# Kernel tuning notes

Hardware: AMD Instinct MI355X
Metric: run time of the kernel (lower is better)

The kernel has to match this reference:

```python
import jax, jax.numpy as jnp
import numpy as np

D = 1024
H = 16
DH = D // H  # 64
EPS = 1e-5


def _ln(x, w, b=None):
    mu = jnp.mean(x, axis=-1, keepdims=True)
    var = jnp.var(x, axis=-1, keepdims=True)
    y = (x - mu) * jax.lax.rsqrt(var + EPS) * w
    return y + b if b is not None else y


def _rotate_half(x):
    x1, x2 = jnp.split(x, 2, axis=-1)
    return jnp.concatenate([-x2, x1], axis=-1)


def _rope(q, k):
    # q, k: [B, L, H, DH]; rotary over sequence dim (ESM-style half-split rotation)
    L = q.shape[1]
    inv_freq = 1.0 / (10000.0 ** (jnp.arange(0, DH, 2, dtype=jnp.float32) / DH))
    freqs = jnp.arange(L, dtype=jnp.float32)[:, None] * inv_freq[None, :]  # [L, DH/2]
    emb = jnp.concatenate([freqs, freqs], axis=-1)  # [L, DH]
    cos = jnp.cos(emb)[None, :, None, :]  # [1, L, 1, DH]
    sin = jnp.sin(emb)[None, :, None, :]
    q = q * cos + _rotate_half(q) * sin
    k = k * cos + _rotate_half(k) * sin
    return q, k


def setup_inputs() -> dict:
    key = jax.random.key(0)
    ks = jax.random.split(key, 8)
    B, L = 2, 2048
    x = jax.random.normal(ks[0], (B, L, D), dtype=jnp.float32)
    seq_id = jnp.sort(jax.random.randint(ks[1], (B, L), 0, 8), axis=-1)
    s = 1.0 / np.sqrt(D)
    return {
        "x": x,
        "seq_id": seq_id,
        "ln1_w": jnp.ones((D,), jnp.float32),
        "ln1_b": jnp.zeros((D,), jnp.float32),
        "w_qkv": jax.random.normal(ks[2], (3 * D, D), dtype=jnp.float32) * s,
        "q_ln_w": jnp.ones((D,), jnp.float32),
        "k_ln_w": jnp.ones((D,), jnp.float32),
        "out_w": jax.random.normal(ks[3], (D, D), dtype=jnp.float32) * s,
    }


def reference(x, seq_id, ln1_w, ln1_b, w_qkv, q_ln_w, k_ln_w, out_w):
    B, L, _ = x.shape
    h = _ln(x, ln1_w, ln1_b)
    qkv = jnp.einsum("bld,ed->ble", h, w_qkv)  # [B, L, 3D]
    q, k, v = jnp.split(qkv, 3, axis=-1)
    q = _ln(q, q_ln_w)
    k = _ln(k, k_ln_w)
    q = q.reshape(B, L, H, DH)
    k = k.reshape(B, L, H, DH)
    q, k = _rope(q, k)
    q = q.transpose(0, 2, 1, 3)  # [B, H, L, DH]
    k = k.transpose(0, 2, 1, 3)
    v = v.reshape(B, L, H, DH).transpose(0, 2, 1, 3)
    scale = 1.0 / np.sqrt(DH)
    scores = jnp.einsum("bhld,bhmd->bhlm", q, k) * scale  # [B, H, L, L]
    mask = (seq_id[:, None, :, None] == seq_id[:, None, None, :])  # [B, 1, L, L]
    scores = jnp.where(mask, scores, -jnp.inf)
    attn = jax.nn.softmax(scores, axis=-1)
    ctx = jnp.einsum("bhlm,bhmd->bhld", attn, v)  # [B, H, L, DH]
    ctx = ctx.transpose(0, 2, 1, 3).reshape(B, L, D)
    return jnp.einsum("bld,ed->ble", ctx, out_w)
```

## Files before the change

kernel.cpp:

```cpp
#include <hip/hip_runtime.h>
#include <hip/hip_bf16.h>
#include <math.h>

#define D 1024
#define H 16
#define DH 64
#define L 2048
#define B 2
#define NROW (B * L)
#define EPS 1e-5f

typedef _Float16 half8 __attribute__((ext_vector_type(8)));
typedef _Float16 half4v __attribute__((ext_vector_type(4)));
typedef float f32x4 __attribute__((ext_vector_type(4)));

__global__ __launch_bounds__(256) void prep_kernel(const float* __restrict__ x,
                                                   const float* __restrict__ lw,
                                                   const float* __restrict__ lb,
                                                   _Float16* __restrict__ h16,
                                                   const float* __restrict__ wqkv,
                                                   _Float16* __restrict__ wqkv16,
                                                   const float* __restrict__ outw,
                                                   _Float16* __restrict__ outw16,
                                                   const int* __restrict__ seq_id,
                                                   int* __restrict__ lo,
                                                   int* __restrict__ hi,
                                                   float2* __restrict__ rtab) {
    int blk = blockIdx.x;
    int t = threadIdx.x;
    if (blk < 4096) {
        int r = blk;
        const float* xr = x + (size_t)r * D;
        float4 v = *(const float4*)&xr[t * 4];
        float s = v.x + v.y + v.z + v.w;
        float sq = v.x * v.x + v.y * v.y + v.z * v.z + v.w * v.w;
        for (int off = 32; off > 0; off >>= 1) {
            s += __shfl_xor(s, off, 64);
            sq += __shfl_xor(sq, off, 64);
        }
        __shared__ float ls[4], lq[4];
        int wave = t >> 6;
        if ((t & 63) == 0) { ls[wave] = s; lq[wave] = sq; }
        __syncthreads();
        float S = ls[0] + ls[1] + ls[2] + ls[3];
        float Q = lq[0] + lq[1] + lq[2] + lq[3];
        float mu = S / (float)D;
        float rs = rsqrtf(Q / (float)D - mu * mu + EPS);
        float4 w4 = *(const float4*)&lw[t * 4];
        float4 b4 = *(const float4*)&lb[t * 4];
        half4v o = {(_Float16)((v.x - mu) * rs * w4.x + b4.x),
                    (_Float16)((v.y - mu) * rs * w4.y + b4.y),
                    (_Float16)((v.z - mu) * rs * w4.z + b4.z),
                    (_Float16)((v.w - mu) * rs * w4.w + b4.w)};
        *(half4v*)&h16[(size_t)r * D + t * 4] = o;
    } else if (blk < 6144) {
        int base = blk - 4096;
        const float* src;
        _Float16* dst;
        if (base < 1536) { src = wqkv; dst = wqkv16; }
        else             { src = outw; dst = outw16; base -= 1536; }
        int i = (base * 256 + t) * 8;
        float4 a = *(const float4*)&src[i];
        float4 b = *(const float4*)&src[i + 4];
        half8 h = {(_Float16)a.x, (_Float16)a.y, (_Float16)a.z, (_Float16)a.w,
                   (_Float16)b.x, (_Float16)b.y, (_Float16)b.z, (_Float16)b.w};
        *(half8*)&dst[i] = h;
    } else if (blk < 6160) {
        int idx = (blk - 6144) * 256 + t;
        int b = idx / L, l = idx - b * L;
        const int* row = seq_id + (size_t)b * L;
        int v = row[l];
        int a = 0, c = L;
        while (a < c) { int m = (a + c) >> 1; if (row[m] < v) a = m + 1; else c = m; }
        lo[idx] = a;
        a = 0; c = L;
        while (a < c) { int m = (a + c) >> 1; if (row[m] <= v) a = m + 1; else c = m; }
        hi[idx] = a;
    } else {
        int idx = (blk - 6160) * 256 + t;
        int l = idx >> 5, fi = idx & 31;
        float invf = expf(-(float)fi * 0.28782313662425572f);
        float sn, cs;
        sincosf((float)l * invf, &sn, &cs);
        rtab[idx] = make_float2(cs, sn);
    }
}

#define LDA_HALF(BUF, MH, DST)                                                      \
    _Pragma("unroll") for (int mt = 0; mt < 4; mt++) {                              \
        int row_ = mw + (MH) * 64 + mt * 16 + col;                                  \
        _Pragma("unroll") for (int kk = 0; kk < 2; kk++)                            \
            DST[mt][kk] = *(const half8*)&As[BUF][row_][((kk * 4 + quad) ^ (row_ & 7)) * 8]; \
    }

#define LDB_HALF(BUF, NH, DST)                                                      \
    _Pragma("unroll") for (int nt = 0; nt < 2; nt++) {                              \
        int row_ = nw + (NH) * 32 + nt * 16 + col;                                  \
        _Pragma("unroll") for (int kk = 0; kk < 2; kk++)                            \
            DST[nt][kk] = *(const half8*)&Bs[BUF][row_][((kk * 4 + quad) ^ (row_ & 7)) * 8]; \
    }

#define MMA_QUAD(MH, NH, AF, BF)                                                    \
    __builtin_amdgcn_s_setprio(1);                                                  \
    _Pragma("unroll") for (int mt = 0; mt < 4; mt++)                                \
    _Pragma("unroll") for (int nt = 0; nt < 2; nt++) {                              \
        acc[(MH) * 4 + mt][(NH) * 2 + nt] = __builtin_amdgcn_mfma_f32_16x16x32_f16( \
            AF[mt][0], BF[nt][0], acc[(MH) * 4 + mt][(NH) * 2 + nt], 0, 0, 0);      \
        acc[(MH) * 4 + mt][(NH) * 2 + nt] = __builtin_amdgcn_mfma_f32_16x16x32_f16( \
            AF[mt][1], BF[nt][1], acc[(MH) * 4 + mt][(NH) * 2 + nt], 0, 0, 0);      \
    }                                                                               \
    __builtin_amdgcn_s_setprio(0);

__global__ __launch_bounds__(512, 2) void gemm1_8phase(const _Float16* __restrict__ A,
                                                       const _Float16* __restrict__ W,
                                                       _Float16* __restrict__ C,
                                                       _Float16* __restrict__ v_t) {
    __shared__ _Float16 As[2][256][64];
    __shared__ _Float16 Bs[2][256][64];
    int t = threadIdx.x;
    int w = t >> 6, lane = t & 63;
    int quad = lane >> 4, col = lane & 15;

    int i = blockIdx.y * 12 + blockIdx.x;
    int xcd = i & 7, j = i >> 3;
    int tm = (xcd >> 1) * 4 + j / 6;
    int tn = (xcd & 1) * 6 + j % 6;
    int m0 = tm * 256, n0 = tn * 256;
    int mw = (w >> 2) * 128, nw = (w & 3) * 64;

    f32x4 acc[8][4] = {};

    auto stageA = [&](int kt, int buf, int half) {
#pragma unroll
        for (int ii = 0; ii < 2; ii++) {
            int e = half * 1024 + ii * 512 + t;
            int row = e >> 3, ch = e & 7;
            int sch = ch ^ (row & 7);
            __builtin_amdgcn_global_load_lds(
                (const __attribute__((address_space(1))) void*)&A[(size_t)(m0 + row) * 1024 + kt * 64 + sch * 8],
                (__attribute__((address_space(3))) void*)&As[buf][row][ch * 8], 16, 0, 0);
        }
    };
    auto stageB = [&](int kt, int buf, int half) {
#pragma unroll
        for (int ii = 0; ii < 2; ii++) {
            int e = half * 1024 + ii * 512 + t;
            int row = e >> 3, ch = e & 7;
            int sch = ch ^ (row & 7);
            __builtin_amdgcn_global_load_lds(
                (const __attribute__((address_space(1))) void*)&W[(size_t)(n0 + row) * 1024 + kt * 64 + sch * 8],
                (__attribute__((address_space(3))) void*)&Bs[buf][row][ch * 8], 16, 0, 0);
        }
    };

    stageA(0, 0, 0); stageA(0, 0, 1); stageB(0, 0, 0); stageB(0, 0, 1);
    stageA(1, 1, 0);
    asm volatile("s_waitcnt vmcnt(2)" ::: "memory");
    __builtin_amdgcn_s_barrier();

    half8 af[4][2], bf0[2][2], bf1[2][2];
    for (int kt = 0; kt < 16; kt++) {
        int p = kt & 1, np = p ^ 1;

        LDA_HALF(p, 0, af);
        LDB_HALF(p, 0, bf0);
        if (kt + 1 < 16) stageA(kt + 1, np, 1);
        __builtin_amdgcn_s_barrier();
        MMA_QUAD(0, 0, af, bf0);
        __builtin_amdgcn_s_barrier();

        LDB_HALF(p, 1, bf1);
        if (kt + 1 < 16) stageB(kt + 1, np, 0);
        __builtin_amdgcn_s_barrier();
        MMA_QUAD(0, 1, af, bf1);
        __builtin_amdgcn_s_barrier();

        LDA_HALF(p, 1, af);
        if (kt + 1 < 16) stageB(kt + 1, np, 1);
        __builtin_amdgcn_s_barrier();
        MMA_QUAD(1, 1, af, bf1);
        __builtin_amdgcn_s_barrier();

        if (kt + 2 < 16) stageA(kt + 2, p, 0);
        MMA_QUAD(1, 0, af, bf0);
        if (kt < 14)       { asm volatile("s_waitcnt vmcnt(2)" ::: "memory"); }
        else if (kt == 14) { asm volatile("s_waitcnt vmcnt(0)" ::: "memory"); }
        if (kt < 15) __builtin_amdgcn_s_barrier();
    }

    if (n0 >= 2048) {
        int b = m0 >> 11;
#pragma unroll
        for (int mt = 0; mt < 8; mt++)
#pragma unroll
            for (int nt = 0; nt < 4; nt++) {
                int vcol = n0 - 2048 + nw + nt * 16 + col;
                int bh = b * H + (vcol >> 6);
                int d = vcol & 63;
                int l = (m0 & (L - 1)) + mw + mt * 16 + quad * 4;
                half4v pk = {(_Float16)acc[mt][nt][0], (_Float16)acc[mt][nt][1],
                             (_Float16)acc[mt][nt][2], (_Float16)acc[mt][nt][3]};
                *(half4v*)&v_t[((size_t)(bh * 64 + d)) * 2048 + l] = pk;
            }
    } else {
#pragma unroll
        for (int mt = 0; mt < 8; mt++)
#pragma unroll
            for (int nt = 0; nt < 4; nt++)
#pragma unroll
                for (int r = 0; r < 4; r++) {
                    int row = m0 + mw + mt * 16 + quad * 4 + r;
                    int cc = n0 + nw + nt * 16 + col;
                    C[(size_t)row * 3072 + cc] = (_Float16)acc[mt][nt][r];
                }
    }
}

template <typename OutT, int BM, int BN>
__global__ __launch_bounds__(256) void gemm_f16_kernel(const _Float16* __restrict__ A,
                                                       const _Float16* __restrict__ W,
                                                       OutT* __restrict__ C, int N) {
    constexpr int WM = BM / 2, WN = BN / 2;
    constexpr int MT = WM / 16, NT = WN / 16;
    __shared__ _Float16 As[2][BM * 32];
    __shared__ _Float16 Bs[2][BN * 32];
    int t = threadIdx.x;
    int w = t >> 6, lane = t & 63;
    int quad = lane >> 4, col = lane & 15;
    int nx = gridDim.x;
    int ib = blockIdx.y * nx + blockIdx.x;
    int nwg = nx * gridDim.y;
    int ni = (ib & 7) * (nwg >> 3) + (ib >> 3);
    int m0 = (ni / nx) * BM, n0 = (ni % nx) * BN;
    int mw = (w >> 1) * WM, nw = (w & 1) * WN;
    int sw = (col >> 1) & 3;

    f32x4 acc[MT][NT] = {};

    auto stage = [&](int k0, int buf) {
#pragma unroll
        for (int i = 0; i < BM / 64; i++) {
            int e = t + i * 256;
            int row = e >> 2, kc = (e & 3) ^ ((row >> 1) & 3);
            __builtin_amdgcn_global_load_lds(
                (const __attribute__((address_space(1))) void*)&A[(size_t)(m0 + row) * 1024 + k0 + kc * 8],
                (__attribute__((address_space(3))) void*)&As[buf][e * 8], 16, 0, 0);
        }
#pragma unroll
        for (int i = 0; i < BN / 64; i++) {
            int e = t + i * 256;
            int row = e >> 2, kc = (e & 3) ^ ((row >> 1) & 3);
            __builtin_amdgcn_global_load_lds(
                (const __attribute__((address_space(1))) void*)&W[(size_t)(n0 + row) * 1024 + k0 + kc * 8],
                (__attribute__((address_space(3))) void*)&Bs[buf][e * 8], 16, 0, 0);
        }
    };

    stage(0, 0);
    int cur = 0;
    for (int k0 = 0; k0 < 1024; k0 += 32) {
        __syncthreads();
        if (k0 + 32 < 1024) stage(k0 + 32, cur ^ 1);
        half8 af[MT], bf[NT];
#pragma unroll
        for (int mt = 0; mt < MT; mt++)
            af[mt] = *(const half8*)&As[cur][(mw + mt * 16 + col) * 32 + ((quad ^ sw) << 3)];
#pragma unroll
        for (int nt = 0; nt < NT; nt++)
            bf[nt] = *(const half8*)&Bs[cur][(nw + nt * 16 + col) * 32 + ((quad ^ sw) << 3)];
#pragma unroll
        for (int mt = 0; mt < MT; mt++)
#pragma unroll
            for (int nt = 0; nt < NT; nt++)
                acc[mt][nt] = __builtin_amdgcn_mfma_f32_16x16x32_f16(af[mt], bf[nt], acc[mt][nt], 0, 0, 0);
        cur ^= 1;
    }

#pragma unroll
    for (int mt = 0; mt < MT; mt++)
#pragma unroll
        for (int nt = 0; nt < NT; nt++)
#pragma unroll
            for (int r = 0; r < 4; r++) {
                int row = m0 + mw + mt * 16 + quad * 4 + r;
                int cc = n0 + nw + nt * 16 + col;
                C[(size_t)row * N + cc] = (OutT)acc[mt][nt][r];
            }
}

__global__ __launch_bounds__(256) void mid_kernel(const _Float16* __restrict__ qkv,
                                                  const float* __restrict__ qw,
                                                  const float* __restrict__ kw,
                                                  const float2* __restrict__ rtab,
                                                  _Float16* __restrict__ q_r,
                                                  _Float16* __restrict__ k_r) {
    __shared__ float ls[4], lq[4];
    int t = threadIdx.x;
    int r = blockIdx.x;
    int half = t >> 7;
    int tt = t & 127;
    const _Float16* src = qkv + (size_t)r * 3072 + half * 1024;
    const float* wgt = half ? kw : qw;
    _Float16* dst = half ? k_r : q_r;

    half8 hv = *(const half8*)&src[tt * 8];
    float y[8];
    float s = 0.f, sq = 0.f;
#pragma unroll
    for (int e = 0; e < 8; e++) {
        float v = (float)hv[e];
        y[e] = v;
        s += v;
        sq += v * v;
    }
    for (int off = 32; off > 0; off >>= 1) {
        s += __shfl_xor(s, off, 64);
        sq += __shfl_xor(sq, off, 64);
    }
    int wave = t >> 6;
    if ((t & 63) == 0) { ls[wave] = s; lq[wave] = sq; }
    __syncthreads();
    int base = half << 1;
    float S = ls[base] + ls[base + 1];
    float Q = lq[base] + lq[base + 1];
    float mu = S / 1024.f;
    float rs = rsqrtf(Q / 1024.f - mu * mu + EPS);

    int l = r & (L - 1);
    int b = r >> 11;
    int j0 = tt * 8;
    int dh0 = j0 & 63, hh = j0 >> 6;
    const float2* cp = &rtab[l * 32 + (dh0 & 31)];
    float4 c01 = *(const float4*)cp;
    float4 c23 = *(const float4*)(cp + 2);
    float4 c45 = *(const float4*)(cp + 4);
    float4 c67 = *(const float4*)(cp + 6);
    float cs_[8] = {c01.x, c01.z, c23.x, c23.z, c45.x, c45.z, c67.x, c67.z};
    float sn_[8] = {c01.y, c01.w, c23.y, c23.w, c45.y, c45.w, c67.y, c67.w};

    float yn[8];
#pragma unroll
    for (int e = 0; e < 8; e++) yn[e] = (y[e] - mu) * rs * wgt[j0 + e];
    float sgn = (dh0 < 32) ? -1.f : 1.f;
    half8 o;
#pragma unroll
    for (int e = 0; e < 8; e++) {
        float p = __shfl_xor(yn[e], 4, 64);
        o[e] = (_Float16)(yn[e] * cs_[e] + sgn * p * sn_[e]);
    }
    *(half8*)&dst[((size_t)((b * H + hh) * L + l)) * 64 + dh0] = o;
}

__global__ __launch_bounds__(512) void attn_mfma_kernel(const _Float16* __restrict__ q_r,
                                                        const _Float16* __restrict__ k_r,
                                                        const _Float16* __restrict__ v_t,
                                                        const int* __restrict__ lo_arr,
                                                        const int* __restrict__ hi_arr,
                                                        _Float16* __restrict__ ctx) {
    __shared__ _Float16 Ks[2][64][64];
    __shared__ _Float16 Vs[2][64][64];
    __shared__ _Float16 Ps[8][16][64];
    int bh = blockIdx.y;
    int b = bh >> 4, h = bh & 15;
    int l0 = blockIdx.x * 128;
    int t = threadIdx.x;
    int w = t >> 6, lane = t & 63;
    int quad = lane >> 4, col = lane & 15;
    int rbase = l0 + w * 16;

    int blo = lo_arr[b * L + l0] & ~63;
    int bhi = hi_arr[b * L + l0 + 127];

    auto stage = [&](int m0, int buf) {
        int row = t >> 3, ch = t & 7;
        int sch = ch ^ (row & 7);
        __builtin_amdgcn_global_load_lds(
            (const __attribute__((address_space(1))) void*)&k_r[((size_t)(bh * L + m0 + row)) * 64 + sch * 8],
            (__attribute__((address_space(3))) void*)&Ks[buf][row][ch * 8], 16, 0, 0);
        __builtin_amdgcn_global_load_lds(
            (const __attribute__((address_space(1))) void*)&v_t[((size_t)(bh * 64 + row)) * 2048 + m0 + sch * 8],
            (__attribute__((address_space(3))) void*)&Vs[buf][row][ch * 8], 16, 0, 0);
    };

    stage(blo, 0);

    half8 qf0, qf1;
    {
        const _Float16* qp = q_r + ((size_t)(bh * L + rbase + col)) * 64 + quad * 8;
        qf0 = *(const half8*)qp;
        qf1 = *(const half8*)(qp + 32);
    }
    int lo_c = lo_arr[b * L + rbase + col];
    int hi_c = hi_arr[b * L + rbase + col];
    int wlo = __shfl(lo_c, 15, 64);
    int whi = __shfl(hi_c, 0, 64);

    f32x4 o[4] = {};
    float m_run = -1e30f, l_run = 0.f;
    const float SCL = 0.125f * 1.4426950408889634f;
    int swz = (col & 7) << 3;
    int src = (lane & 48) | ((lane & 48) >> 2);

    int cur = 0;
    for (int m0 = blo; m0 < bhi; m0 += 64) {
        __syncthreads();
        if (m0 + 64 < bhi) stage(m0 + 64, cur ^ 1);

        f32x4 s[4] = {};
#pragma unroll
        for (int nt = 0; nt < 4; nt++) {
            int key = nt * 16 + col;
            const _Float16* kp = &Ks[cur][key][0];
            half8 kf0 = *(const half8*)&kp[(quad ^ (key & 7)) * 8];
            half8 kf1 = *(const half8*)&kp[((quad + 4) ^ (key & 7)) * 8];
            s[nt] = __builtin_amdgcn_mfma_f32_16x16x32_f16(kf0, qf0, s[nt], 0, 0, 0);
            s[nt] = __builtin_amdgcn_mfma_f32_16x16x32_f16(kf1, qf1, s[nt], 0, 0, 0);
        }

        float p[4][4];
        bool full = (m0 >= wlo) && (m0 + 64 <= whi);
        if (full) {
#pragma unroll
            for (int nt = 0; nt < 4; nt++)
#pragma unroll
                for (int r = 0; r < 4; r++) p[nt][r] = s[nt][r] * SCL;
        } else {
#pragma unroll
            for (int nt = 0; nt < 4; nt++) {
                int kb = m0 + nt * 16 + quad * 4;
#pragma unroll
                for (int r = 0; r < 4; r++) {
                    int key = kb + r;
                    p[nt][r] = (key >= lo_c && key < hi_c) ? s[nt][r] * SCL : -INFINITY;
                }
            }
        }

        float tmax = p[0][0];
#pragma unroll
        for (int nt = 0; nt < 4; nt++)
#pragma unroll
            for (int r = 0; r < 4; r++) tmax = fmaxf(tmax, p[nt][r]);
        tmax = fmaxf(tmax, __shfl_xor(tmax, 16, 64));
        tmax = fmaxf(tmax, __shfl_xor(tmax, 32, 64));
        float nm = fmaxf(m_run, tmax);
        float corr = exp2f(m_run - nm);
        m_run = nm;
        float rs = 0.f;
#pragma unroll
        for (int nt = 0; nt < 4; nt++)
#pragma unroll
            for (int r = 0; r < 4; r++) {
                float e2 = exp2f(p[nt][r] - nm);
                p[nt][r] = e2;
                rs += e2;
            }
        rs += __shfl_xor(rs, 16, 64);
        rs += __shfl_xor(rs, 32, 64);
        l_run = l_run * corr + rs;

#pragma unroll
        for (int nt = 0; nt < 4; nt++) {
            half4v pk = {(_Float16)p[nt][0], (_Float16)p[nt][1],
                         (_Float16)p[nt][2], (_Float16)p[nt][3]};
            *(half4v*)&Ps[w][col][(nt * 16 + quad * 4) ^ swz] = pk;
        }

#pragma unroll
        for (int r = 0; r < 4; r++) {
            float c4 = __shfl(corr, src + r, 64);
            o[0][r] *= c4; o[1][r] *= c4; o[2][r] *= c4; o[3][r] *= c4;
        }

        half8 pf0 = *(const half8*)&Ps[w][col][(quad * 8) ^ swz];
        half8 pf1 = *(const half8*)&Ps[w][col][(32 + quad * 8) ^ swz];
#pragma unroll
        for (int nt = 0; nt < 4; nt++) {
            int dr = nt * 16 + col;
            const _Float16* vp = &Vs[cur][dr][0];
            half8 vf0 = *(const half8*)&vp[(quad ^ (dr & 7)) * 8];
            half8 vf1 = *(const half8*)&vp[((quad + 4) ^ (dr & 7)) * 8];
            o[nt] = __builtin_amdgcn_mfma_f32_16x16x32_f16(pf0, vf0, o[nt], 0, 0, 0);
            o[nt] = __builtin_amdgcn_mfma_f32_16x16x32_f16(pf1, vf1, o[nt], 0, 0, 0);
        }
        cur ^= 1;
    }

#pragma unroll
    for (int r = 0; r < 4; r++) {
        float linv = 1.f / __shfl(l_run, src + r, 64);
        int row = rbase + quad * 4 + r;
#pragma unroll
        for (int nt = 0; nt < 4; nt++)
            ctx[((size_t)(b * L + row)) * 1024 + h * 64 + nt * 16 + col] =
                (_Float16)(o[nt][r] * linv);
    }
}

extern "C" void kernel_launch(void* const* d_in, const int* in_sizes, int n_in,
                              void* d_out, int out_size, void* d_ws, size_t ws_size,
                              hipStream_t stream) {
    const float* x      = (const float*)d_in[0];
    const int*   seq_id = (const int*)d_in[1];
    const float* ln1_w  = (const float*)d_in[2];
    const float* ln1_b  = (const float*)d_in[3];
    const float* w_qkv  = (const float*)d_in[4];
    const float* q_ln_w = (const float*)d_in[5];
    const float* k_ln_w = (const float*)d_in[6];
    const float* out_w  = (const float*)d_in[7];
    float* out = (float*)d_out;

    char* ws = (char*)d_ws;
    int*      lo     = (int*)(ws);
    int*      hi     = (int*)(ws + (64 << 10));
    float2*   rtab   = (float2*)(ws + (128 << 10));
    _Float16* h16    = (_Float16*)(ws + (1ull << 20));
    _Float16* wqkv16 = (_Float16*)(ws + (10ull << 20));
    _Float16* outw16 = (_Float16*)(ws + (17ull << 20));
    _Float16* qkv16  = (_Float16*)(ws + (20ull << 20));
    _Float16* q_r    = (_Float16*)(ws + (45ull << 20));
    _Float16* k_r    = (_Float16*)(ws + (54ull << 20));
    _Float16* v_t    = (_Float16*)(ws + (63ull << 20));
    _Float16* ctx16  = (_Float16*)(ws + (72ull << 20));

    prep_kernel<<<dim3(6416), dim3(256), 0, stream>>>(
        x, ln1_w, ln1_b, h16, w_qkv, wqkv16, out_w, outw16, seq_id, lo, hi, rtab);
    gemm1_8phase<<<dim3(12, 16), dim3(512), 0, stream>>>(h16, wqkv16, qkv16, v_t);
    mid_kernel<<<dim3(4096), dim3(256), 0, stream>>>(qkv16, q_ln_w, k_ln_w, rtab, q_r, k_r);
    attn_mfma_kernel<<<dim3(L / 128, B * H), dim3(512), 0, stream>>>(q_r, k_r, v_t, lo, hi, ctx16);
    gemm_f16_kernel<float, 128, 64><<<dim3(1024 / 64, NROW / 128), dim3(256), 0, stream>>>(
        ctx16, outw16, out, 1024);

    (void)in_sizes; (void)n_in; (void)out_size; (void)ws_size;
}
```

Baseline: 184.5 us.

## Interleave warp tile quadrants and restage GEMM1 prefetch to load by quadrant

Result: no change. 186.4 us (+1.1%).

```diff
diff --git a/kernel.cpp b/kernel.cpp
--- a/kernel.cpp
+++ b/kernel.cpp
@@ -88,14 +88,14 @@
 
 #define LDA_HALF(BUF, MH, DST)                                                      \
     _Pragma("unroll") for (int mt = 0; mt < 4; mt++) {                              \
-        int row_ = mw + (MH) * 64 + mt * 16 + col;                                  \
+        int row_ = (MH) * 128 + mw + mt * 16 + col;                                 \
         _Pragma("unroll") for (int kk = 0; kk < 2; kk++)                            \
             DST[mt][kk] = *(const half8*)&As[BUF][row_][((kk * 4 + quad) ^ (row_ & 7)) * 8]; \
     }
 
 #define LDB_HALF(BUF, NH, DST)                                                      \
     _Pragma("unroll") for (int nt = 0; nt < 2; nt++) {                              \
-        int row_ = nw + (NH) * 32 + nt * 16 + col;                                  \
+        int row_ = (NH) * 128 + nw + nt * 16 + col;                                 \
         _Pragma("unroll") for (int kk = 0; kk < 2; kk++)                            \
             DST[nt][kk] = *(const half8*)&Bs[BUF][row_][((kk * 4 + quad) ^ (row_ & 7)) * 8]; \
     }
@@ -126,7 +126,7 @@
     int tm = (xcd >> 1) * 4 + j / 6;
     int tn = (xcd & 1) * 6 + j % 6;
     int m0 = tm * 256, n0 = tn * 256;
-    int mw = (w >> 2) * 128, nw = (w & 3) * 64;
+    int mw = (w >> 2) * 64, nw = (w & 3) * 32;
 
     f32x4 acc[8][4] = {};
 
@@ -153,39 +153,42 @@
         }
     };
 
-    stageA(0, 0, 0); stageA(0, 0, 1); stageB(0, 0, 0); stageB(0, 0, 1);
-    stageA(1, 1, 0);
-    asm volatile("s_waitcnt vmcnt(2)" ::: "memory");
+    stageA(0, 0, 0); stageB(0, 0, 0); stageB(0, 0, 1); stageA(0, 0, 1);
+    asm volatile("s_waitcnt vmcnt(4)" ::: "memory");
     __builtin_amdgcn_s_barrier();
 
     half8 af[4][2], bf0[2][2], bf1[2][2];
     for (int kt = 0; kt < 16; kt++) {
         int p = kt & 1, np = p ^ 1;
+        bool more = (kt + 1) < 16;
 
         LDA_HALF(p, 0, af);
         LDB_HALF(p, 0, bf0);
-        if (kt + 1 < 16) stageA(kt + 1, np, 1);
+        if (more) stageA(kt + 1, np, 0);
         __builtin_amdgcn_s_barrier();
         MMA_QUAD(0, 0, af, bf0);
+        if (more) { asm volatile("s_waitcnt vmcnt(4)" ::: "memory"); }
+        else      { asm volatile("s_waitcnt vmcnt(2)" ::: "memory"); }
         __builtin_amdgcn_s_barrier();
 
         LDB_HALF(p, 1, bf1);
-        if (kt + 1 < 16) stageB(kt + 1, np, 0);
+        if (more) stageB(kt + 1, np, 0);
         __builtin_amdgcn_s_barrier();
         MMA_QUAD(0, 1, af, bf1);
+        if (more) { asm volatile("s_waitcnt vmcnt(4)" ::: "memory"); }
+        else      { asm volatile("s_waitcnt vmcnt(0)" ::: "memory"); }
         __builtin_amdgcn_s_barrier();
 
         LDA_HALF(p, 1, af);
-        if (kt + 1 < 16) stageB(kt + 1, np, 1);
+        if (more) stageB(kt + 1, np, 1);
         __builtin_amdgcn_s_barrier();
         MMA_QUAD(1, 1, af, bf1);
         __builtin_amdgcn_s_barrier();
 
-        if (kt + 2 < 16) stageA(kt + 2, p, 0);
+        if (more) stageA(kt + 1, np, 1);
         MMA_QUAD(1, 0, af, bf0);
-        if (kt < 14)       { asm volatile("s_waitcnt vmcnt(2)" ::: "memory"); }
-        else if (kt == 14) { asm volatile("s_waitcnt vmcnt(0)" ::: "memory"); }
-        if (kt < 15) __builtin_amdgcn_s_barrier();
+        if (more) { asm volatile("s_waitcnt vmcnt(4)" ::: "memory"); }
+        __builtin_amdgcn_s_barrier();
     }
 
     if (n0 >= 2048) {
@@ -194,10 +197,10 @@
         for (int mt = 0; mt < 8; mt++)
 #pragma unroll
             for (int nt = 0; nt < 4; nt++) {
-                int vcol = n0 - 2048 + nw + nt * 16 + col;
+                int vcol = n0 - 2048 + (nt >> 1) * 128 + nw + (nt & 1) * 16 + col;
                 int bh = b * H + (vcol >> 6);
                 int d = vcol & 63;
-                int l = (m0 & (L - 1)) + mw + mt * 16 + quad * 4;
+                int l = (m0 & (L - 1)) + (mt >> 2) * 128 + mw + (mt & 3) * 16 + quad * 4;
                 half4v pk = {(_Float16)acc[mt][nt][0], (_Float16)acc[mt][nt][1],
                              (_Float16)acc[mt][nt][2], (_Float16)acc[mt][nt][3]};
                 *(half4v*)&v_t[((size_t)(bh * 64 + d)) * 2048 + l] = pk;
@@ -209,8 +212,8 @@
             for (int nt = 0; nt < 4; nt++)
 #pragma unroll
                 for (int r = 0; r < 4; r++) {
-                    int row = m0 + mw + mt * 16 + quad * 4 + r;
-                    int cc = n0 + nw + nt * 16 + col;
+                    int row = m0 + (mt >> 2) * 128 + mw + (mt & 3) * 16 + quad * 4 + r;
+                    int cc = n0 + (nt >> 1) * 128 + nw + (nt & 1) * 16 + col;
                     C[(size_t)row * 3072 + cc] = (_Float16)acc[mt][nt][r];
                 }
     }
```
